# Kernel optimization log

Measured on AMD Instinct MI355X. Metric: run time of the kernel, lower is better.

## Reference

```python
import jax, jax.numpy as jnp
import numpy as np

SAMP_RATE = 24000
HARMONIC_NUM = 8
DIM = HARMONIC_NUM + 1
SINE_AMP = 0.1
NOISE_STD = 0.003
VOICED_THRESHOLD = 0.0
B, L = 16, 240000


def setup_inputs() -> dict:
    key = jax.random.key(0)
    k_f0, k_voiced, k_ini, k_noise, k_w = jax.random.split(key, 5)
    f0 = jax.random.uniform(k_f0, (B, L, 1), jnp.float32, 80.0, 400.0)
    voiced = (jax.random.uniform(k_voiced, (B, L, 1)) > 0.2).astype(jnp.float32)
    f0 = f0 * voiced
    # random initial phase per (batch, harmonic); fundamental gets phase 0
    rand_ini = jax.random.uniform(k_ini, (B, DIM), jnp.float32)
    rand_ini = rand_ini.at[:, 0].set(0.0)
    noise = jax.random.normal(k_noise, (B, L, DIM), jnp.float32)
    merge_w = jax.random.normal(k_w, (1, DIM), jnp.float32) / np.sqrt(DIM)
    return {"f0": f0, "rand_ini": rand_ini, "noise": noise, "merge_w": merge_w}


def reference(f0, rand_ini, noise, merge_w):
    # f0_buf: fundamental plus harmonics -> (B, L, DIM)
    harmonics = jnp.arange(1, DIM + 1, dtype=f0.dtype)  # [1, 2, ..., DIM]
    f0_buf = f0 * harmonics  # broadcast (B,L,1)*(DIM,)

    # normalized instantaneous frequency in cycles/sample, with random init phase
    rad_values = jnp.mod(f0_buf / SAMP_RATE, 1.0)
    rad_values = rad_values.at[:, 0, :].add(rand_ini)

    # phase-wrap correction: detect where cumsum%1 wraps, subtract 1 there
    tmp_over_one = jnp.mod(jnp.cumsum(rad_values, axis=1), 1.0)
    wrap = (tmp_over_one[:, 1:, :] - tmp_over_one[:, :-1, :]) < 0
    cumsum_shift = jnp.concatenate(
        [jnp.zeros_like(rad_values[:, :1, :]), -wrap.astype(rad_values.dtype)], axis=1
    )
    phase = jnp.cumsum(rad_values + cumsum_shift, axis=1)
    sine_waves = jnp.sin(phase * (2.0 * jnp.pi)) * SINE_AMP

    # voiced/unvoiced mask and noise injection
    uv = (f0 > VOICED_THRESHOLD).astype(f0.dtype)  # (B, L, 1)
    noise_amp = uv * NOISE_STD + (1.0 - uv) * (SINE_AMP / 3.0)
    sine_waves = sine_waves * uv + noise_amp * noise

    # merge: Linear(DIM, 1, bias=False) + tanh
    out = jnp.tanh(jnp.einsum("bld,od->blo", sine_waves, merge_w))
    return out
```

## Files before the change

### kernel.cpp

```cpp
#include <hip/hip_runtime.h>
#include <math.h>

namespace {
constexpr int kB = 16;
constexpr int kL = 240000;
constexpr int kD = 9;
constexpr float kInvSamp = 1.0f / 24000.0f;
constexpr int kChunk = 2048;
constexpr int kT = 8;
constexpr int kThreads = 256;
constexpr int kNChunks = 118;
constexpr float kSineAmp = 0.1f;
constexpr float kNoiseStd = 0.003f;
constexpr float kNoiseUnv = (float)(0.1 / 3.0);
}

__global__ __launch_bounds__(kThreads) void sine_pass_a(
    const float* __restrict__ f0, double* __restrict__ agg) {
  const int c = blockIdx.x, b = blockIdx.y, tid = threadIdx.x;
  const int l0 = c * kChunk + tid * kT;
  float s = 0.0f;
  if (l0 < kL) {
    const float4* f4 = reinterpret_cast<const float4*>(f0 + (size_t)b * kL + l0);
    const float4 a = f4[0], bb = f4[1];
    s = ((a.x + a.y) + (a.z + a.w)) + ((bb.x + bb.y) + (bb.z + bb.w));
  }
  __shared__ double red[kThreads];
  red[tid] = (double)s * (double)kInvSamp;
  __syncthreads();
  for (int ofs = kThreads / 2; ofs > 0; ofs >>= 1) {
    if (tid < ofs) red[tid] += red[tid + ofs];
    __syncthreads();
  }
  if (tid == 0) agg[(size_t)b * kNChunks + c] = red[0];
}

__global__ __launch_bounds__(kThreads) void sine_emit(
    const float* __restrict__ f0, const float* __restrict__ rand_ini,
    const float* __restrict__ noise, const float* __restrict__ w,
    const double* __restrict__ agg, float* __restrict__ out) {
  __shared__ double sc[kThreads];
  __shared__ double red[kThreads];
  const int c = blockIdx.x, b = blockIdx.y, tid = threadIdx.x;
  const int l0 = c * kChunk + tid * kT;
  const bool active = l0 < kL;

  float rq[kT];
  float tsum = 0.0f;
  if (active) {
    const float4* f4 = reinterpret_cast<const float4*>(f0 + (size_t)b * kL + l0);
    const float4 a = f4[0], bb = f4[1];
    rq[0] = a.x * kInvSamp; rq[1] = a.y * kInvSamp;
    rq[2] = a.z * kInvSamp; rq[3] = a.w * kInvSamp;
    rq[4] = bb.x * kInvSamp; rq[5] = bb.y * kInvSamp;
    rq[6] = bb.z * kInvSamp; rq[7] = bb.w * kInvSamp;
#pragma unroll
    for (int j = 0; j < kT; ++j) tsum += rq[j];
  } else {
#pragma unroll
    for (int j = 0; j < kT; ++j) rq[j] = 0.0f;
  }

  float nz[kT * kD];
  if (active) {
    const float4* n4 =
        reinterpret_cast<const float4*>(noise + ((size_t)b * kL + l0) * kD);
#pragma unroll
    for (int i = 0; i < 18; ++i) {
      const float4 x = n4[i];
      nz[4 * i + 0] = x.x; nz[4 * i + 1] = x.y;
      nz[4 * i + 2] = x.z; nz[4 * i + 3] = x.w;
    }
  }

  red[tid] = (tid < c) ? agg[(size_t)b * kNChunks + tid] : 0.0;
  __syncthreads();
  for (int ofs = kThreads / 2; ofs > 0; ofs >>= 1) {
    if (tid < ofs) red[tid] += red[tid + ofs];
    __syncthreads();
  }
  const double base = red[0];

  sc[tid] = (double)tsum;
  __syncthreads();
  for (int ofs = 1; ofs < kThreads; ofs <<= 1) {
    const double u = (tid >= ofs) ? sc[tid - ofs] : 0.0;
    __syncthreads();
    sc[tid] += u;
    __syncthreads();
  }

  if (!active) return;

  const double cbase = base + sc[tid] - (double)tsum;

  float basef[kD], wv[kD];
#pragma unroll
  for (int d = 0; d < kD; ++d) {
    const double ph = (double)(d + 1) * cbase + (double)rand_ini[b * kD + d];
    basef[d] = (float)(ph - floor(ph));
    wv[d] = w[d];
  }

  float ob[kT];
  float pref = 0.0f;
#pragma unroll
  for (int j = 0; j < kT; ++j) {
    pref += rq[j];
    const float f = rq[j];
    const float au = (f > 0.0f) ? kSineAmp : 0.0f;
    const float namp = (f > 0.0f) ? kNoiseStd : kNoiseUnv;
    float dots = 0.0f, dotn = 0.0f;
#pragma unroll
    for (int d = 0; d < kD; ++d) {
      const float pf = __builtin_amdgcn_fractf(basef[d] + (float)(d + 1) * pref);
      const float sv = __builtin_amdgcn_sinf(pf);
      dots = fmaf(wv[d], sv, dots);
      dotn = fmaf(wv[d], nz[j * kD + d], dotn);
    }
    const float x = au * dots + namp * dotn;
    const float e = __expf(2.0f * x);
    ob[j] = 1.0f - 2.0f * __builtin_amdgcn_rcpf(e + 1.0f);
  }

  float4* o4 = reinterpret_cast<float4*>(out + (size_t)b * kL + l0);
  o4[0] = make_float4(ob[0], ob[1], ob[2], ob[3]);
  o4[1] = make_float4(ob[4], ob[5], ob[6], ob[7]);
}

extern "C" void kernel_launch(void* const* d_in, const int* in_sizes, int n_in,
                              void* d_out, int out_size, void* d_ws,
                              size_t ws_size, hipStream_t stream) {
  const float* f0 = (const float*)d_in[0];
  const float* rand_ini = (const float*)d_in[1];
  const float* noise = (const float*)d_in[2];
  const float* w = (const float*)d_in[3];
  float* out = (float*)d_out;
  double* agg = (double*)d_ws;

  const dim3 grid(kNChunks, kB), block(kThreads);
  sine_pass_a<<<grid, block, 0, stream>>>(f0, agg);
  sine_emit<<<grid, block, 0, stream>>>(f0, rand_ini, noise, w, agg, out);
}
```

Baseline: 35.85 us.

## Replace shared-memory reductions and scans with wavefront shuffles, nontemporal noise loads

```diff
diff --git a/kernel.cpp b/kernel.cpp
--- a/kernel.cpp
+++ b/kernel.cpp
@@ -13,6 +13,7 @@
 constexpr float kSineAmp = 0.1f;
 constexpr float kNoiseStd = 0.003f;
 constexpr float kNoiseUnv = (float)(0.1 / 3.0);
+typedef float vfloat4 __attribute__((ext_vector_type(4)));
 }
 
 __global__ __launch_bounds__(kThreads) void sine_pass_a(
@@ -25,23 +26,22 @@
     const float4 a = f4[0], bb = f4[1];
     s = ((a.x + a.y) + (a.z + a.w)) + ((bb.x + bb.y) + (bb.z + bb.w));
   }
-  __shared__ double red[kThreads];
-  red[tid] = (double)s * (double)kInvSamp;
+  double v = (double)s * (double)kInvSamp;
+#pragma unroll
+  for (int ofs = 1; ofs < 64; ofs <<= 1) v += __shfl_xor(v, ofs, 64);
+  __shared__ double wt[4];
+  const int wid = tid >> 6;
+  if ((tid & 63) == 0) wt[wid] = v;
   __syncthreads();
-  for (int ofs = kThreads / 2; ofs > 0; ofs >>= 1) {
-    if (tid < ofs) red[tid] += red[tid + ofs];
-    __syncthreads();
-  }
-  if (tid == 0) agg[(size_t)b * kNChunks + c] = red[0];
+  if (tid == 0) agg[(size_t)b * kNChunks + c] = wt[0] + wt[1] + wt[2] + wt[3];
 }
 
 __global__ __launch_bounds__(kThreads) void sine_emit(
     const float* __restrict__ f0, const float* __restrict__ rand_ini,
     const float* __restrict__ noise, const float* __restrict__ w,
     const double* __restrict__ agg, float* __restrict__ out) {
-  __shared__ double sc[kThreads];
-  __shared__ double red[kThreads];
   const int c = blockIdx.x, b = blockIdx.y, tid = threadIdx.x;
+  const int lane = tid & 63, wid = tid >> 6;
   const int l0 = c * kChunk + tid * kT;
   const bool active = l0 < kL;
 
@@ -61,38 +61,38 @@
     for (int j = 0; j < kT; ++j) rq[j] = 0.0f;
   }
 
-  float nz[kT * kD];
+  double pv = (tid < c) ? agg[(size_t)b * kNChunks + tid] : 0.0;
+
+  vfloat4 nzv[18];
   if (active) {
-    const float4* n4 =
-        reinterpret_cast<const float4*>(noise + ((size_t)b * kL + l0) * kD);
+    const vfloat4* n4 =
+        reinterpret_cast<const vfloat4*>(noise + ((size_t)b * kL + l0) * kD);
 #pragma unroll
-    for (int i = 0; i < 18; ++i) {
-      const float4 x = n4[i];
-      nz[4 * i + 0] = x.x; nz[4 * i + 1] = x.y;
-      nz[4 * i + 2] = x.z; nz[4 * i + 3] = x.w;
-    }
+    for (int i = 0; i < 18; ++i) nzv[i] = __builtin_nontemporal_load(n4 + i);
   }
 
-  red[tid] = (tid < c) ? agg[(size_t)b * kNChunks + tid] : 0.0;
+#pragma unroll
+  for (int ofs = 1; ofs < 64; ofs <<= 1) pv += __shfl_xor(pv, ofs, 64);
+
+  double incl = (double)tsum;
+#pragma unroll
+  for (int ofs = 1; ofs < 64; ofs <<= 1) {
+    const double u = __shfl_up(incl, ofs, 64);
+    if (lane >= ofs) incl += u;
+  }
+
+  __shared__ double rtot[4], wtot[4];
+  if (lane == 0) rtot[wid] = pv;
+  if (lane == 63) wtot[wid] = incl;
   __syncthreads();
-  for (int ofs = kThreads / 2; ofs > 0; ofs >>= 1) {
-    if (tid < ofs) red[tid] += red[tid + ofs];
-    __syncthreads();
-  }
-  const double base = red[0];
-
-  sc[tid] = (double)tsum;
-  __syncthreads();
-  for (int ofs = 1; ofs < kThreads; ofs <<= 1) {
-    const double u = (tid >= ofs) ? sc[tid - ofs] : 0.0;
-    __syncthreads();
-    sc[tid] += u;
-    __syncthreads();
-  }
 
   if (!active) return;
 
-  const double cbase = base + sc[tid] - (double)tsum;
+  double base = rtot[0] + rtot[1] + rtot[2] + rtot[3];
+#pragma unroll
+  for (int k = 0; k < 4; ++k)
+    if (k < wid) base += wtot[k];
+  const double cbase = base + incl - (double)tsum;
 
   float basef[kD], wv[kD];
 #pragma unroll
@@ -102,23 +102,31 @@
     wv[d] = w[d];
   }
 
-  float ob[kT];
+  float dots[kT];
   float pref = 0.0f;
 #pragma unroll
   for (int j = 0; j < kT; ++j) {
     pref += rq[j];
+    float s = 0.0f;
+#pragma unroll
+    for (int d = 0; d < kD; ++d) {
+      const float pf = __builtin_amdgcn_fractf(basef[d] + (float)(d + 1) * pref);
+      s = fmaf(wv[d], __builtin_amdgcn_sinf(pf), s);
+    }
+    dots[j] = s;
+  }
+
+  const float* nz = reinterpret_cast<const float*>(nzv);
+  float ob[kT];
+#pragma unroll
+  for (int j = 0; j < kT; ++j) {
     const float f = rq[j];
     const float au = (f > 0.0f) ? kSineAmp : 0.0f;
     const float namp = (f > 0.0f) ? kNoiseStd : kNoiseUnv;
-    float dots = 0.0f, dotn = 0.0f;
+    float dotn = 0.0f;
 #pragma unroll
-    for (int d = 0; d < kD; ++d) {
-      const float pf = __builtin_amdgcn_fractf(basef[d] + (float)(d + 1) * pref);
-      const float sv = __builtin_amdgcn_sinf(pf);
-      dots = fmaf(wv[d], sv, dots);
-      dotn = fmaf(wv[d], nz[j * kD + d], dotn);
-    }
-    const float x = au * dots + namp * dotn;
+    for (int d = 0; d < kD; ++d) dotn = fmaf(wv[d], nz[j * kD + d], dotn);
+    const float x = au * dots[j] + namp * dotn;
     const float e = __expf(2.0f * x);
     ob[j] = 1.0f - 2.0f * __builtin_amdgcn_rcpf(e + 1.0f);
   }
```

Measured after the change: 92.61 us. +158.3%, slower.
